# Performance work log

Measured on AMD Instinct MI355X. Metric: run time of the kernel, lower is better.

The kernel has to match this reference:

```python
import jax, jax.numpy as jnp
import numpy as np

# Problem sizes
B, NPG, K = 64, 1024, 16          # graphs, nodes-per-graph, kNN neighbors
IN_CH, OUT_CH, SPACE, PROP = 64, 128, 4, 64
N = B * NPG


def setup_inputs() -> dict:
    key = jax.random.key(0)
    ks = jax.random.split(key, 10)

    def lin(k, out_d, in_d):
        return jax.random.normal(k, (out_d, in_d), jnp.float32) / np.sqrt(in_d)

    x = jax.random.normal(ks[0], (N, IN_CH), jnp.float32)
    z = jax.random.normal(ks[1], (N,), jnp.float32)
    batch = (jnp.arange(N) // NPG).astype(jnp.int32)  # 64 equal graphs
    return {
        "x": x,
        "z": z,
        "batch": batch,
        "Ws": lin(ks[2], SPACE, IN_CH),
        "bs": jnp.zeros((SPACE,), jnp.float32),
        "Wh": lin(ks[3], PROP, IN_CH),
        "bh": jnp.zeros((PROP,), jnp.float32),
        "Wskip": lin(ks[4], OUT_CH, IN_CH),
        "Wagg": lin(ks[5], OUT_CH, 4 * PROP),
        "bagg": jnp.zeros((OUT_CH,), jnp.float32),
        "gamma": jnp.ones((OUT_CH,), jnp.float32),
        "beta": jnp.zeros((OUT_CH,), jnp.float32),
    }


def reference(x, z, batch, Ws, bs, Wh, bh, Wskip, Wagg, bagg, gamma, beta):
    # --- linear projections (torch Linear: y = x @ W.T + b) ---
    s = x @ Ws.T + bs                              # [N, SPACE] learned space
    h = x @ Wh.T + bh                              # [N, PROP]  propagated feats

    sB = s.reshape(B, NPG, SPACE)
    hB = h.reshape(B, NPG, PROP)
    zB = z.reshape(B, NPG)

    # --- exact kNN per graph (knn_graph with batch, no self-loops) ---
    sq = jnp.sum(sB * sB, -1)                      # [B, n]
    d2 = sq[:, :, None] + sq[:, None, :] - 2.0 * jnp.einsum("bnd,bmd->bnm", sB, sB)
    d2 = jnp.where(jnp.eye(NPG, dtype=bool), jnp.inf, d2)  # exclude self
    _, idx = jax.lax.top_k(-d2, K)                 # idx[b, i, :] = k nearest j
    idx = jax.lax.stop_gradient(idx)

    gather = jax.vmap(lambda a, i: a[i])           # per-graph row gather

    # --- edge weights ew = exp(-10 * ||s_src - s_dst||^2) ---
    s_nb = gather(sB, idx)                         # [B, n, K, SPACE]
    ew = jnp.exp(-10.0 * jnp.sum((s_nb - sB[:, :, None, :]) ** 2, -1))  # [B,n,K]

    # --- messages m = h[src] * ew ; each dst has exactly K incoming edges ---
    m = gather(hB, idx) * ew[..., None]            # [B, n, K, PROP]
    agg_mean = m.mean(axis=2)                      # scatter_mean
    agg_max = m.max(axis=2)                        # scatter_max

    # --- DGN directional aggregations over Z ---
    dz = gather(zB, idx) - zB[:, :, None]          # z[src] - z[dst], [B,n,K]
    dz_abs_sum = jnp.sum(jnp.abs(dz), axis=2)      # scatter_sum(|dz|), [B,n]
    F = dz / (dz_abs_sum[:, :, None] + 1e-8)       # [B, n, K]
    agg_smooth = (m * jnp.abs(F)[..., None]).mean(axis=2)
    agg_deriv = (m * F[..., None]).sum(axis=2)

    agg = jnp.concatenate([agg_mean, agg_max, agg_smooth, agg_deriv], -1)
    agg = agg.reshape(N, 4 * PROP)

    out = x @ Wskip.T + (agg @ Wagg.T + bagg)      # [N, OUT_CH]

    # --- BatchNorm1d (training-mode batch stats, biased var) + ReLU ---
    mu = out.mean(axis=0)
    var = out.var(axis=0)
    out = gamma * (out - mu) * jax.lax.rsqrt(var + 1e-5) + beta
    return jax.nn.relu(out)
```

## Files before the change

### kernel.cpp

```cpp
#include <hip/hip_runtime.h>
#include <hip/hip_bf16.h>
#include <math.h>

#define NPG   1024
#define KNN   16
#define IN_CH 64
#define OUT_CH 128
#define SPACE 4
#define PROP  64
#define NGRAPH 64
#define NTOT  (NGRAPH*NPG)

typedef unsigned long long u64;
typedef unsigned int u32;

#define K_INF ((0xFF800000ULL << 32) | 0x3FFULL)

__global__ __launch_bounds__(256) void k1_proj(
    const float* __restrict__ x, const float* __restrict__ Ws, const float* __restrict__ bs,
    const float* __restrict__ Wh, const float* __restrict__ bh,
    float* __restrict__ s_out, float* __restrict__ h_out)
{
    __shared__ float whl[PROP*IN_CH];
    __shared__ float wsl[SPACE*IN_CH];
    int tid = threadIdx.x;
    {
        const float4* src = (const float4*)Wh;
        float4* dst = (float4*)whl;
        for (int e = tid; e < PROP*IN_CH/4; e += 256) dst[e] = src[e];
        if (tid < SPACE*IN_CH/4) ((float4*)wsl)[tid] = ((const float4*)Ws)[tid];
    }
    __syncthreads();
    int i = blockIdx.x*256 + tid;

    float4 xr[16];
    const float4* xrow = (const float4*)(x + (size_t)i*IN_CH);
    #pragma unroll
    for (int q = 0; q < 16; q++) xr[q] = xrow[q];

    #pragma unroll
    for (int d = 0; d < SPACE; d++) {
        float acc = bs[d];
        const float4* wr = (const float4*)(wsl + d*IN_CH);
        #pragma unroll
        for (int q = 0; q < 16; q++) {
            float4 w = wr[q];
            acc += xr[q].x*w.x + xr[q].y*w.y + xr[q].z*w.z + xr[q].w*w.w;
        }
        s_out[(size_t)i*SPACE + d] = acc;
    }
    #pragma unroll 4
    for (int p = 0; p < PROP; p++) {
        float acc = bh[p];
        const float4* wr = (const float4*)(whl + p*IN_CH);
        #pragma unroll
        for (int q = 0; q < 16; q++) {
            float4 w = wr[q];
            acc += xr[q].x*w.x + xr[q].y*w.y + xr[q].z*w.z + xr[q].w*w.w;
        }
        h_out[(size_t)i*PROP + p] = acc;
    }
}

#define CEU(a,b) { u64 _lo=(a)<(b)?(a):(b); u64 _hi=(a)<(b)?(b):(a); (a)=_lo; (b)=_hi; }
#define CED(a,b) { u64 _lo=(a)<(b)?(a):(b); u64 _hi=(a)<(b)?(b):(a); (a)=_hi; (b)=_lo; }

#define M16N(n0,n1,n2,n3,n4,n5,n6,n7,n8,n9,n10,n11,n12,n13,n14,n15) \
 CEU(n0,n8) CEU(n1,n9) CEU(n2,n10) CEU(n3,n11) CEU(n4,n12) CEU(n5,n13) CEU(n6,n14) CEU(n7,n15) \
 CEU(n0,n4) CEU(n1,n5) CEU(n2,n6) CEU(n3,n7) CEU(n8,n12) CEU(n9,n13) CEU(n10,n14) CEU(n11,n15) \
 CEU(n0,n2) CEU(n1,n3) CEU(n4,n6) CEU(n5,n7) CEU(n8,n10) CEU(n9,n11) CEU(n12,n14) CEU(n13,n15) \
 CEU(n0,n1) CEU(n2,n3) CEU(n4,n5) CEU(n6,n7) CEU(n8,n9) CEU(n10,n11) CEU(n12,n13) CEU(n14,n15)

#define S16N(n0,n1,n2,n3,n4,n5,n6,n7,n8,n9,n10,n11,n12,n13,n14,n15) \
 CEU(n0,n1) CED(n2,n3) CEU(n4,n5) CED(n6,n7) CEU(n8,n9) CED(n10,n11) CEU(n12,n13) CED(n14,n15) \
 CEU(n0,n2) CEU(n1,n3) CED(n4,n6) CED(n5,n7) CEU(n8,n10) CEU(n9,n11) CED(n12,n14) CED(n13,n15) \
 CEU(n0,n1) CEU(n2,n3) CED(n4,n5) CED(n6,n7) CEU(n8,n9) CEU(n10,n11) CED(n12,n13) CED(n14,n15) \
 CEU(n0,n4) CEU(n1,n5) CEU(n2,n6) CEU(n3,n7) CED(n8,n12) CED(n9,n13) CED(n10,n14) CED(n11,n15) \
 CEU(n0,n2) CEU(n1,n3) CEU(n4,n6) CEU(n5,n7) CED(n8,n10) CED(n9,n11) CED(n12,n14) CED(n13,n15) \
 CEU(n0,n1) CEU(n2,n3) CED(n4,n5) CED(n6,n7) CEU(n8,n9) CEU(n10,n11) CED(n12,n13) CED(n14,n15) \
 M16N(n0,n1,n2,n3,n4,n5,n6,n7,n8,n9,n10,n11,n12,n13,n14,n15)

__device__ __forceinline__ float unmono(u32 uw) {
    return __uint_as_float((uw & 0x80000000u) ? (uw & 0x7FFFFFFFu) : ~uw);
}

#define POPN(b, dst) { \
    int _jb = (int)(q0 & 1023u); \
    q0 = (q0 >> 10) | (q1 << 54); q1 = (q1 >> 10) | (q2 << 54); q2 >>= 10; \
    float4 _sb = s4[_jb]; \
    float _dx = si.x-_sb.x, _dy = si.y-_sb.y, _dz = si.z-_sb.z, _dw = si.w-_sb.w; \
    float _db = _dx*_dx + _dy*_dy + _dz*_dz + _dw*_dw; \
    u32 _u = __float_as_uint(_db); _u = (_u >> 31) ? ~_u : (_u | 0x80000000u); \
    dst = ((b) < cnt) ? ((((u64)_u) << 32) | (u32)_jb) : ~0ULL; \
}

#define FLUSHK() do{ \
    u64 n0,n1,n2,n3,n4,n5,n6,n7,n8,n9,n10,n11,n12,n13,n14,n15; \
    POPN(0,n0) POPN(1,n1) POPN(2,n2) POPN(3,n3) POPN(4,n4) POPN(5,n5) POPN(6,n6) POPN(7,n7) \
    POPN(8,n8) POPN(9,n9) POPN(10,n10) POPN(11,n11) POPN(12,n12) POPN(13,n13) POPN(14,n14) POPN(15,n15) \
    S16N(n0,n1,n2,n3,n4,n5,n6,n7,n8,n9,n10,n11,n12,n13,n14,n15) \
    kk0 =kk0 <n15?kk0 :n15; kk1 =kk1 <n14?kk1 :n14; kk2 =kk2 <n13?kk2 :n13; kk3 =kk3 <n12?kk3 :n12; \
    kk4 =kk4 <n11?kk4 :n11; kk5 =kk5 <n10?kk5 :n10; kk6 =kk6 <n9 ?kk6 :n9 ; kk7 =kk7 <n8 ?kk7 :n8 ; \
    kk8 =kk8 <n7 ?kk8 :n7 ; kk9 =kk9 <n6 ?kk9 :n6 ; kk10=kk10<n5 ?kk10:n5 ; kk11=kk11<n4 ?kk11:n4 ; \
    kk12=kk12<n3 ?kk12:n3 ; kk13=kk13<n2 ?kk13:n2 ; kk14=kk14<n1 ?kk14:n1 ; kk15=kk15<n0 ?kk15:n0 ; \
    M16N(kk0,kk1,kk2,kk3,kk4,kk5,kk6,kk7,kk8,kk9,kk10,kk11,kk12,kk13,kk14,kk15) \
    cnt = 0; \
    wf = unmono((u32)(kk15 >> 32)); \
}while(0)

#define SHF64(v,mm) ((u64)__shfl_xor((long long)(v), (mm)))
#define MRG(mm) do{ \
    u64 p0=SHF64(kk15,mm), p1=SHF64(kk14,mm), p2 =SHF64(kk13,mm), p3 =SHF64(kk12,mm); \
    u64 p4=SHF64(kk11,mm), p5=SHF64(kk10,mm), p6 =SHF64(kk9,mm),  p7 =SHF64(kk8,mm); \
    u64 p8=SHF64(kk7,mm),  p9=SHF64(kk6,mm),  p10=SHF64(kk5,mm),  p11=SHF64(kk4,mm); \
    u64 p12=SHF64(kk3,mm), p13=SHF64(kk2,mm), p14=SHF64(kk1,mm),  p15=SHF64(kk0,mm); \
    kk0 =kk0 <p0 ?kk0 :p0 ; kk1 =kk1 <p1 ?kk1 :p1 ; kk2 =kk2 <p2 ?kk2 :p2 ; kk3 =kk3 <p3 ?kk3 :p3 ; \
    kk4 =kk4 <p4 ?kk4 :p4 ; kk5 =kk5 <p5 ?kk5 :p5 ; kk6 =kk6 <p6 ?kk6 :p6 ; kk7 =kk7 <p7 ?kk7 :p7 ; \
    kk8 =kk8 <p8 ?kk8 :p8 ; kk9 =kk9 <p9 ?kk9 :p9 ; kk10=kk10<p10?kk10:p10; kk11=kk11<p11?kk11:p11; \
    kk12=kk12<p12?kk12:p12; kk13=kk13<p13?kk13:p13; kk14=kk14<p14?kk14:p14; kk15=kk15<p15?kk15:p15; \
    M16N(kk0,kk1,kk2,kk3,kk4,kk5,kk6,kk7,kk8,kk9,kk10,kk11,kk12,kk13,kk14,kk15) \
}while(0)

#define OUTE(e, kv) if (((e) & 3) == r) { \
    int _j = (int)((kv) & 1023u); \
    float _d2 = unmono((u32)((kv) >> 32)); \
    ew_out[bq + (e)] = expf(-10.0f * _d2); \
    idx_out[bq + (e)] = gbase + _j; }

__attribute__((amdgpu_waves_per_eu(4, 4)))
__global__ __launch_bounds__(256) void k2_knn(
    const float* __restrict__ s, int* __restrict__ idx_out, float* __restrict__ ew_out)
{
    __shared__ float4 s4[NPG];
    int tid = threadIdx.x;
    int g    = blockIdx.x >> 4;
    int gbase = g * NPG;
    int qblk = (blockIdx.x & 15) * 64;
    const float4* sg = (const float4*)(s + (size_t)g*NPG*SPACE);
    for (int e = tid; e < NPG; e += 256) s4[e] = sg[e];
    __syncthreads();

    int lane = tid & 63;
    int grp  = lane >> 2;
    int r    = lane & 3;
    int q    = qblk + (tid >> 6)*16 + grp;
    float4 si = s4[q];

    u64 kk0=K_INF,kk1=K_INF,kk2=K_INF,kk3=K_INF,kk4=K_INF,kk5=K_INF,kk6=K_INF,kk7=K_INF,
        kk8=K_INF,kk9=K_INF,kk10=K_INF,kk11=K_INF,kk12=K_INF,kk13=K_INF,kk14=K_INF,kk15=K_INF;
    float wf = INFINITY;
    int cnt = 0;
    u64 q0 = 0, q1 = 0, q2 = 0;

    #pragma unroll 1
    for (int it = 0; it < 256; ++it) {
        int j = r*256 + ((it + 61*r) & 255);
        float4 sj = s4[j];
        float dx = si.x-sj.x, dy = si.y-sj.y, dz = si.z-sj.z, dw = si.w-sj.w;
        float d2 = dx*dx + dy*dy + dz*dz + dw*dw;
        if ((d2 <= wf) && (j != q)) {
            q2 = (q2 << 10) | (q1 >> 54);
            q1 = (q1 << 10) | (q0 >> 54);
            q0 = (q0 << 10) | (u32)j;
            cnt++;
        }
        if (__any(cnt >= 16)) FLUSHK();
    }
    if (__any(cnt > 0)) FLUSHK();

    MRG(1);
    MRG(2);

    size_t bq = ((size_t)(gbase + q)) * KNN;
    OUTE(0,kk0)  OUTE(1,kk1)  OUTE(2,kk2)  OUTE(3,kk3)
    OUTE(4,kk4)  OUTE(5,kk5)  OUTE(6,kk6)  OUTE(7,kk7)
    OUTE(8,kk8)  OUTE(9,kk9)  OUTE(10,kk10) OUTE(11,kk11)
    OUTE(12,kk12) OUTE(13,kk13) OUTE(14,kk14) OUTE(15,kk15)
}

typedef __attribute__((ext_vector_type(8))) short bf16x8;
typedef __attribute__((ext_vector_type(4))) float f32x4;

__device__ __forceinline__ u32 pk2bf(float a, float b) {
    u32 ua = __float_as_uint(a);
    u32 ub = __float_as_uint(b);
    ua = (ua + 0x7fffu + ((ua >> 16) & 1u)) >> 16;
    ub = (ub + 0x7fffu + ((ub >> 16) & 1u)) >> 16;
    return (ua & 0xffffu) | (ub << 16);
}
__device__ __forceinline__ unsigned short bfr(float a) {
    u32 ua = __float_as_uint(a);
    ua = (ua + 0x7fffu + ((ua >> 16) & 1u)) >> 16;
    return (unsigned short)ua;
}

__global__ __launch_bounds__(256) void k34_agg_gemm(
    const float* __restrict__ x, const float* __restrict__ h,
    const float* __restrict__ z, const int* __restrict__ idx,
    const float* __restrict__ ew,
    const float* __restrict__ Wskip, const float* __restrict__ Wagg,
    const float* __restrict__ bagg, float* __restrict__ out,
    float* __restrict__ partial)
{
    __shared__ char AggL[64*512];
    __shared__ char Bl[128*128];
    __shared__ float st[128], st2[128];
    int tid = threadIdx.x;
    int lane = tid & 63, wid = tid >> 6;
    int bid = blockIdx.x;
    int tile = (bid & 7) * 128 + (bid >> 3);
    int mbase = tile * 64;

    if (tid < 128) { st[tid] = 0.f; st2[tid] = 0.f; }

    #pragma unroll 2
    for (int t = 0; t < 16; ++t) {
        int row = wid*16 + t;
        int node = mbase + row;
        int kq = lane & 15;
        int jv = idx[(size_t)node*KNN + kq];
        float ev = ew[(size_t)node*KNN + kq];
        float dz = z[jv] - z[node];
        float as = fabsf(dz);
        as += __shfl_xor(as, 1); as += __shfl_xor(as, 2);
        as += __shfl_xor(as, 4); as += __shfl_xor(as, 8);
        float F = dz / (as + 1e-8f);
        float mean = 0.f, mx = -INFINITY, sm = 0.f, dv = 0.f;
        #pragma unroll
        for (int k = 0; k < KNN; ++k) {
            int   j = __shfl(jv, k);
            float e = __shfl(ev, k);
            float f = __shfl(F,  k);
            float hv = h[(size_t)j*PROP + lane];
            float m = hv * e;
            mean += m; mx = fmaxf(mx, m);
            sm += m * fabsf(f); dv += m * f;
        }
        int swz = (row & 7) << 4;
        char* rp = AggL + row*512;
        *(unsigned short*)(rp + ((2*(lane      )) ^ swz)) = bfr(mean * 0.0625f);
        *(unsigned short*)(rp + ((2*(lane +  64)) ^ swz)) = bfr(mx);
        *(unsigned short*)(rp + ((2*(lane + 128)) ^ swz)) = bfr(sm * 0.0625f);
        *(unsigned short*)(rp + ((2*(lane + 192)) ^ swz)) = bfr(dv);
    }

    int wy = wid >> 1, wx = wid & 1;
    int colb = wx*64 + (lane & 15);
    f32x4 acc[2][4];
    #pragma unroll
    for (int nc = 0; nc < 4; ++nc) {
        float bv = bagg[colb + nc*16];
        #pragma unroll
        for (int mr = 0; mr < 2; ++mr) acc[mr][nc] = (f32x4){bv, bv, bv, bv};
    }

    int brow = tid >> 1, bkq = (tid & 1) * 32;
    int bsw = (brow & 7) << 4;

    for (int ch = 0; ch < 5; ++ch) {
        __syncthreads();
        const float* bp = (ch == 0) ? (Wskip + (size_t)brow*64  + bkq)
                                    : (Wagg  + (size_t)brow*256 + (ch-1)*64 + bkq);
        #pragma unroll
        for (int g2 = 0; g2 < 4; ++g2) {
            float4 f0 = ((const float4*)bp)[2*g2], f1 = ((const float4*)bp)[2*g2+1];
            uint4 u = { pk2bf(f0.x,f0.y), pk2bf(f0.z,f0.w), pk2bf(f1.x,f1.y), pk2bf(f1.z,f1.w) };
            *(uint4*)(Bl + brow*128 + ((bkq*2 + g2*16) ^ bsw)) = u;
        }
        __syncthreads();

        #pragma unroll
        for (int ks = 0; ks < 2; ++ks) {
            int kb = ks*64 + ((lane >> 4) * 16);
            bf16x8 af[2], bfrg[4];
            if (ch == 0) {
                int ke = ks*32 + (lane >> 4)*8;
                #pragma unroll
                for (int mr = 0; mr < 2; ++mr) {
                    int row = mbase + wy*32 + mr*16 + (lane & 15);
                    const float* xp = x + (size_t)row*64 + ke;
                    float4 f0 = *(const float4*)xp, f1 = *(const float4*)(xp + 4);
                    union { u32 u[4]; bf16x8 v; } cv;
                    cv.u[0] = pk2bf(f0.x,f0.y); cv.u[1] = pk2bf(f0.z,f0.w);
                    cv.u[2] = pk2bf(f1.x,f1.y); cv.u[3] = pk2bf(f1.z,f1.w);
                    af[mr] = cv.v;
                }
            } else {
                #pragma unroll
                for (int mr = 0; mr < 2; ++mr) {
                    int row = wy*32 + mr*16 + (lane & 15);
                    af[mr] = *(const bf16x8*)(AggL + row*512 + (ch-1)*128
                                              + (kb ^ ((row & 7) << 4)));
                }
            }
            #pragma unroll
            for (int nc = 0; nc < 4; ++nc) {
                int n = wx*64 + nc*16 + (lane & 15);
                bfrg[nc] = *(const bf16x8*)(Bl + n*128 + (kb ^ ((n & 7) << 4)));
            }
            #pragma unroll
            for (int mr = 0; mr < 2; ++mr)
                #pragma unroll
                for (int nc = 0; nc < 4; ++nc)
                    acc[mr][nc] = __builtin_amdgcn_mfma_f32_16x16x32_bf16(
                        af[mr], bfrg[nc], acc[mr][nc], 0, 0, 0);
        }
    }

    float s1[4] = {0,0,0,0}, s2[4] = {0,0,0,0};
    #pragma unroll
    for (int mr = 0; mr < 2; ++mr) {
        int r0 = mbase + wy*32 + mr*16 + (lane >> 4)*4;
        #pragma unroll
        for (int nc = 0; nc < 4; ++nc) {
            int c = colb + nc*16;
            #pragma unroll
            for (int j = 0; j < 4; ++j) {
                float v = acc[mr][nc][j];
                out[(size_t)(r0 + j)*OUT_CH + c] = v;
                s1[nc] += v;
                s2[nc] += v*v;
            }
        }
    }
    #pragma unroll
    for (int nc = 0; nc < 4; ++nc) {
        s1[nc] += __shfl_xor(s1[nc], 16); s1[nc] += __shfl_xor(s1[nc], 32);
        s2[nc] += __shfl_xor(s2[nc], 16); s2[nc] += __shfl_xor(s2[nc], 32);
    }
    __syncthreads();
    if ((lane >> 4) == 0) {
        #pragma unroll
        for (int nc = 0; nc < 4; ++nc) {
            atomicAdd(&st[colb + nc*16],  s1[nc]);
            atomicAdd(&st2[colb + nc*16], s2[nc]);
        }
    }
    __syncthreads();
    if (tid < 128) {
        partial[(size_t)bid*256 + tid]       = st[tid];
        partial[(size_t)bid*256 + 128 + tid] = st2[tid];
    }
}

__global__ __launch_bounds__(256) void k5_red(
    const float* __restrict__ partial, float* __restrict__ sums)
{
    int c = threadIdx.x;
    int b0 = blockIdx.x * 32;
    float acc = 0.f;
    #pragma unroll 8
    for (int b = 0; b < 32; ++b)
        acc += partial[(size_t)(b0 + b)*256 + c];
    atomicAdd(&sums[c], acc);
}

__global__ __launch_bounds__(256) void k6_bn(
    float* __restrict__ out, const float* __restrict__ sums,
    const float* __restrict__ gamma, const float* __restrict__ beta)
{
    int f = blockIdx.x*256 + threadIdx.x;
    float4 v = *(float4*)(out + (size_t)f*4);
    int o0 = (f*4) & 127;
    const float invN = 1.f / (float)NTOT;
    float r[4] = {v.x, v.y, v.z, v.w};
    #pragma unroll
    for (int c = 0; c < 4; c++) {
        int o = o0 + c;
        float mu  = sums[o] * invN;
        float var = sums[128+o] * invN - mu*mu;
        float sc  = gamma[o] * rsqrtf(var + 1e-5f);
        float sh  = beta[o] - mu*sc;
        float y = r[c]*sc + sh;
        r[c] = y > 0.f ? y : 0.f;
    }
    *(float4*)(out + (size_t)f*4) = make_float4(r[0], r[1], r[2], r[3]);
}

extern "C" void kernel_launch(void* const* d_in, const int* in_sizes, int n_in,
                              void* d_out, int out_size, void* d_ws, size_t ws_size,
                              hipStream_t stream)
{
    (void)in_sizes; (void)n_in; (void)out_size; (void)ws_size;
    const float* x     = (const float*)d_in[0];
    const float* z     = (const float*)d_in[1];
    const float* Ws    = (const float*)d_in[3];
    const float* bs    = (const float*)d_in[4];
    const float* Wh    = (const float*)d_in[5];
    const float* bh    = (const float*)d_in[6];
    const float* Wskip = (const float*)d_in[7];
    const float* Wagg  = (const float*)d_in[8];
    const float* bagg  = (const float*)d_in[9];
    const float* gamma = (const float*)d_in[10];
    const float* beta  = (const float*)d_in[11];
    float* out = (float*)d_out;

    const size_t N = NTOT;
    float* ws   = (float*)d_ws;
    float* sbuf = ws;
    float* hbuf = sbuf + N*4;
    int*   idxb = (int*)(hbuf + N*64);
    float* ewb  = (float*)(idxb + N*16);
    float* part = ewb + N*16;
    float* sums = part + 1024*256;

    hipMemsetAsync(sums, 0, 256*sizeof(float), stream);
    k1_proj<<<NTOT/256, 256, 0, stream>>>(x, Ws, bs, Wh, bh, sbuf, hbuf);
    k2_knn <<<NGRAPH*16, 256, 0, stream>>>(sbuf, idxb, ewb);
    k34_agg_gemm<<<NTOT/64, 256, 0, stream>>>(x, hbuf, z, idxb, ewb,
                                              Wskip, Wagg, bagg, out, part);
    k5_red<<<32, 256, 0, stream>>>(part, sums);
    k6_bn <<<NTOT*OUT_CH/4/256, 256, 0, stream>>>(out, sums, gamma, beta);
}
```

Before: 315.4 us.

## Replace filtered bitonic top-k with 32-bit packed-key med3 insertion network

```diff
diff --git a/kernel.cpp b/kernel.cpp
--- a/kernel.cpp
+++ b/kernel.cpp
@@ -14,8 +14,6 @@
 typedef unsigned long long u64;
 typedef unsigned int u32;
 
-#define K_INF ((0xFF800000ULL << 32) | 0x3FFULL)
-
 __global__ __launch_bounds__(256) void k1_proj(
     const float* __restrict__ x, const float* __restrict__ Ws, const float* __restrict__ bs,
     const float* __restrict__ Wh, const float* __restrict__ bh,
@@ -62,120 +60,92 @@
     }
 }
 
-#define CEU(a,b) { u64 _lo=(a)<(b)?(a):(b); u64 _hi=(a)<(b)?(b):(a); (a)=_lo; (b)=_hi; }
-#define CED(a,b) { u64 _lo=(a)<(b)?(a):(b); u64 _hi=(a)<(b)?(b):(a); (a)=_hi; (b)=_lo; }
-
-#define M16N(n0,n1,n2,n3,n4,n5,n6,n7,n8,n9,n10,n11,n12,n13,n14,n15) \
- CEU(n0,n8) CEU(n1,n9) CEU(n2,n10) CEU(n3,n11) CEU(n4,n12) CEU(n5,n13) CEU(n6,n14) CEU(n7,n15) \
- CEU(n0,n4) CEU(n1,n5) CEU(n2,n6) CEU(n3,n7) CEU(n8,n12) CEU(n9,n13) CEU(n10,n14) CEU(n11,n15) \
- CEU(n0,n2) CEU(n1,n3) CEU(n4,n6) CEU(n5,n7) CEU(n8,n10) CEU(n9,n11) CEU(n12,n14) CEU(n13,n15) \
- CEU(n0,n1) CEU(n2,n3) CEU(n4,n5) CEU(n6,n7) CEU(n8,n9) CEU(n10,n11) CEU(n12,n13) CEU(n14,n15)
-
-#define S16N(n0,n1,n2,n3,n4,n5,n6,n7,n8,n9,n10,n11,n12,n13,n14,n15) \
- CEU(n0,n1) CED(n2,n3) CEU(n4,n5) CED(n6,n7) CEU(n8,n9) CED(n10,n11) CEU(n12,n13) CED(n14,n15) \
- CEU(n0,n2) CEU(n1,n3) CED(n4,n6) CED(n5,n7) CEU(n8,n10) CEU(n9,n11) CED(n12,n14) CED(n13,n15) \
- CEU(n0,n1) CEU(n2,n3) CED(n4,n5) CED(n6,n7) CEU(n8,n9) CEU(n10,n11) CED(n12,n13) CED(n14,n15) \
- CEU(n0,n4) CEU(n1,n5) CEU(n2,n6) CEU(n3,n7) CED(n8,n12) CED(n9,n13) CED(n10,n14) CED(n11,n15) \
- CEU(n0,n2) CEU(n1,n3) CEU(n4,n6) CEU(n5,n7) CED(n8,n10) CED(n9,n11) CED(n12,n14) CED(n13,n15) \
- CEU(n0,n1) CEU(n2,n3) CED(n4,n5) CED(n6,n7) CEU(n8,n9) CEU(n10,n11) CED(n12,n13) CED(n14,n15) \
- M16N(n0,n1,n2,n3,n4,n5,n6,n7,n8,n9,n10,n11,n12,n13,n14,n15)
-
-__device__ __forceinline__ float unmono(u32 uw) {
-    return __uint_as_float((uw & 0x80000000u) ? (uw & 0x7FFFFFFFu) : ~uw);
-}
-
-#define POPN(b, dst) { \
-    int _jb = (int)(q0 & 1023u); \
-    q0 = (q0 >> 10) | (q1 << 54); q1 = (q1 >> 10) | (q2 << 54); q2 >>= 10; \
-    float4 _sb = s4[_jb]; \
-    float _dx = si.x-_sb.x, _dy = si.y-_sb.y, _dz = si.z-_sb.z, _dw = si.w-_sb.w; \
-    float _db = _dx*_dx + _dy*_dy + _dz*_dz + _dw*_dw; \
-    u32 _u = __float_as_uint(_db); _u = (_u >> 31) ? ~_u : (_u | 0x80000000u); \
-    dst = ((b) < cnt) ? ((((u64)_u) << 32) | (u32)_jb) : ~0ULL; \
-}
-
-#define FLUSHK() do{ \
-    u64 n0,n1,n2,n3,n4,n5,n6,n7,n8,n9,n10,n11,n12,n13,n14,n15; \
-    POPN(0,n0) POPN(1,n1) POPN(2,n2) POPN(3,n3) POPN(4,n4) POPN(5,n5) POPN(6,n6) POPN(7,n7) \
-    POPN(8,n8) POPN(9,n9) POPN(10,n10) POPN(11,n11) POPN(12,n12) POPN(13,n13) POPN(14,n14) POPN(15,n15) \
-    S16N(n0,n1,n2,n3,n4,n5,n6,n7,n8,n9,n10,n11,n12,n13,n14,n15) \
-    kk0 =kk0 <n15?kk0 :n15; kk1 =kk1 <n14?kk1 :n14; kk2 =kk2 <n13?kk2 :n13; kk3 =kk3 <n12?kk3 :n12; \
-    kk4 =kk4 <n11?kk4 :n11; kk5 =kk5 <n10?kk5 :n10; kk6 =kk6 <n9 ?kk6 :n9 ; kk7 =kk7 <n8 ?kk7 :n8 ; \
-    kk8 =kk8 <n7 ?kk8 :n7 ; kk9 =kk9 <n6 ?kk9 :n6 ; kk10=kk10<n5 ?kk10:n5 ; kk11=kk11<n4 ?kk11:n4 ; \
-    kk12=kk12<n3 ?kk12:n3 ; kk13=kk13<n2 ?kk13:n2 ; kk14=kk14<n1 ?kk14:n1 ; kk15=kk15<n0 ?kk15:n0 ; \
-    M16N(kk0,kk1,kk2,kk3,kk4,kk5,kk6,kk7,kk8,kk9,kk10,kk11,kk12,kk13,kk14,kk15) \
-    cnt = 0; \
-    wf = unmono((u32)(kk15 >> 32)); \
+#define MED3(d, x, a, b) asm("v_med3_u32 %0, %1, %2, %3" : "=v"(d) : "v"(x), "v"(a), "v"(b))
+#define UMIN(a,b) ((a)<(b)?(a):(b))
+
+#define INS16(x) do{ \
+    u32 _x = (x); \
+    MED3(kk15, _x, kk14, kk15); MED3(kk14, _x, kk13, kk14); \
+    MED3(kk13, _x, kk12, kk13); MED3(kk12, _x, kk11, kk12); \
+    MED3(kk11, _x, kk10, kk11); MED3(kk10, _x, kk9,  kk10); \
+    MED3(kk9,  _x, kk8,  kk9 ); MED3(kk8,  _x, kk7,  kk8 ); \
+    MED3(kk7,  _x, kk6,  kk7 ); MED3(kk6,  _x, kk5,  kk6 ); \
+    MED3(kk5,  _x, kk4,  kk5 ); MED3(kk4,  _x, kk3,  kk4 ); \
+    MED3(kk3,  _x, kk2,  kk3 ); MED3(kk2,  _x, kk1,  kk2 ); \
+    MED3(kk1,  _x, kk0,  kk1 ); kk0 = UMIN(_x, kk0); \
 }while(0)
 
-#define SHF64(v,mm) ((u64)__shfl_xor((long long)(v), (mm)))
-#define MRG(mm) do{ \
-    u64 p0=SHF64(kk15,mm), p1=SHF64(kk14,mm), p2 =SHF64(kk13,mm), p3 =SHF64(kk12,mm); \
-    u64 p4=SHF64(kk11,mm), p5=SHF64(kk10,mm), p6 =SHF64(kk9,mm),  p7 =SHF64(kk8,mm); \
-    u64 p8=SHF64(kk7,mm),  p9=SHF64(kk6,mm),  p10=SHF64(kk5,mm),  p11=SHF64(kk4,mm); \
-    u64 p12=SHF64(kk3,mm), p13=SHF64(kk2,mm), p14=SHF64(kk1,mm),  p15=SHF64(kk0,mm); \
-    kk0 =kk0 <p0 ?kk0 :p0 ; kk1 =kk1 <p1 ?kk1 :p1 ; kk2 =kk2 <p2 ?kk2 :p2 ; kk3 =kk3 <p3 ?kk3 :p3 ; \
-    kk4 =kk4 <p4 ?kk4 :p4 ; kk5 =kk5 <p5 ?kk5 :p5 ; kk6 =kk6 <p6 ?kk6 :p6 ; kk7 =kk7 <p7 ?kk7 :p7 ; \
-    kk8 =kk8 <p8 ?kk8 :p8 ; kk9 =kk9 <p9 ?kk9 :p9 ; kk10=kk10<p10?kk10:p10; kk11=kk11<p11?kk11:p11; \
-    kk12=kk12<p12?kk12:p12; kk13=kk13<p13?kk13:p13; kk14=kk14<p14?kk14:p14; kk15=kk15<p15?kk15:p15; \
-    M16N(kk0,kk1,kk2,kk3,kk4,kk5,kk6,kk7,kk8,kk9,kk10,kk11,kk12,kk13,kk14,kk15) \
+#define CEU32(a,b) { u32 _lo = UMIN(a,b); u32 _hi = (a)<(b)?(b):(a); (a)=_lo; (b)=_hi; }
+#define M16U(n0,n1,n2,n3,n4,n5,n6,n7,n8,n9,n10,n11,n12,n13,n14,n15) \
+ CEU32(n0,n8) CEU32(n1,n9) CEU32(n2,n10) CEU32(n3,n11) CEU32(n4,n12) CEU32(n5,n13) CEU32(n6,n14) CEU32(n7,n15) \
+ CEU32(n0,n4) CEU32(n1,n5) CEU32(n2,n6) CEU32(n3,n7) CEU32(n8,n12) CEU32(n9,n13) CEU32(n10,n14) CEU32(n11,n15) \
+ CEU32(n0,n2) CEU32(n1,n3) CEU32(n4,n6) CEU32(n5,n7) CEU32(n8,n10) CEU32(n9,n11) CEU32(n12,n14) CEU32(n13,n15) \
+ CEU32(n0,n1) CEU32(n2,n3) CEU32(n4,n5) CEU32(n6,n7) CEU32(n8,n9) CEU32(n10,n11) CEU32(n12,n13) CEU32(n14,n15)
+
+#define MRGU(mm) do{ \
+    u32 p0 =(u32)__shfl_xor((int)kk15,mm), p1 =(u32)__shfl_xor((int)kk14,mm); \
+    u32 p2 =(u32)__shfl_xor((int)kk13,mm), p3 =(u32)__shfl_xor((int)kk12,mm); \
+    u32 p4 =(u32)__shfl_xor((int)kk11,mm), p5 =(u32)__shfl_xor((int)kk10,mm); \
+    u32 p6 =(u32)__shfl_xor((int)kk9, mm), p7 =(u32)__shfl_xor((int)kk8, mm); \
+    u32 p8 =(u32)__shfl_xor((int)kk7, mm), p9 =(u32)__shfl_xor((int)kk6, mm); \
+    u32 p10=(u32)__shfl_xor((int)kk5, mm), p11=(u32)__shfl_xor((int)kk4, mm); \
+    u32 p12=(u32)__shfl_xor((int)kk3, mm), p13=(u32)__shfl_xor((int)kk2, mm); \
+    u32 p14=(u32)__shfl_xor((int)kk1, mm), p15=(u32)__shfl_xor((int)kk0, mm); \
+    kk0 =UMIN(kk0 ,p0 ); kk1 =UMIN(kk1 ,p1 ); kk2 =UMIN(kk2 ,p2 ); kk3 =UMIN(kk3 ,p3 ); \
+    kk4 =UMIN(kk4 ,p4 ); kk5 =UMIN(kk5 ,p5 ); kk6 =UMIN(kk6 ,p6 ); kk7 =UMIN(kk7 ,p7 ); \
+    kk8 =UMIN(kk8 ,p8 ); kk9 =UMIN(kk9 ,p9 ); kk10=UMIN(kk10,p10); kk11=UMIN(kk11,p11); \
+    kk12=UMIN(kk12,p12); kk13=UMIN(kk13,p13); kk14=UMIN(kk14,p14); kk15=UMIN(kk15,p15); \
+    M16U(kk0,kk1,kk2,kk3,kk4,kk5,kk6,kk7,kk8,kk9,kk10,kk11,kk12,kk13,kk14,kk15) \
 }while(0)
 
-#define OUTE(e, kv) if (((e) & 3) == r) { \
+#define OUTE8(e, kv) if (((e) & 7) == r) { \
     int _j = (int)((kv) & 1023u); \
-    float _d2 = unmono((u32)((kv) >> 32)); \
+    float4 _sj = s4[_j]; \
+    float _dx = si.x-_sj.x, _dy = si.y-_sj.y, _dz = si.z-_sj.z, _dw = si.w-_sj.w; \
+    float _d2 = _dx*_dx + _dy*_dy + _dz*_dz + _dw*_dw; \
     ew_out[bq + (e)] = expf(-10.0f * _d2); \
     idx_out[bq + (e)] = gbase + _j; }
 
-__attribute__((amdgpu_waves_per_eu(4, 4)))
 __global__ __launch_bounds__(256) void k2_knn(
     const float* __restrict__ s, int* __restrict__ idx_out, float* __restrict__ ew_out)
 {
     __shared__ float4 s4[NPG];
     int tid = threadIdx.x;
-    int g    = blockIdx.x >> 4;
+    int g     = blockIdx.x >> 5;
     int gbase = g * NPG;
-    int qblk = (blockIdx.x & 15) * 64;
+    int qblk  = (blockIdx.x & 31) * 32;
     const float4* sg = (const float4*)(s + (size_t)g*NPG*SPACE);
     for (int e = tid; e < NPG; e += 256) s4[e] = sg[e];
     __syncthreads();
 
     int lane = tid & 63;
-    int grp  = lane >> 2;
-    int r    = lane & 3;
-    int q    = qblk + (tid >> 6)*16 + grp;
+    int grp  = lane >> 3;
+    int r    = lane & 7;
+    int q    = qblk + (tid >> 6)*8 + grp;
     float4 si = s4[q];
 
-    u64 kk0=K_INF,kk1=K_INF,kk2=K_INF,kk3=K_INF,kk4=K_INF,kk5=K_INF,kk6=K_INF,kk7=K_INF,
-        kk8=K_INF,kk9=K_INF,kk10=K_INF,kk11=K_INF,kk12=K_INF,kk13=K_INF,kk14=K_INF,kk15=K_INF;
-    float wf = INFINITY;
-    int cnt = 0;
-    u64 q0 = 0, q1 = 0, q2 = 0;
-
-    #pragma unroll 1
-    for (int it = 0; it < 256; ++it) {
-        int j = r*256 + ((it + 61*r) & 255);
+    u32 kk0=~0u,kk1=~0u,kk2=~0u,kk3=~0u,kk4=~0u,kk5=~0u,kk6=~0u,kk7=~0u,
+        kk8=~0u,kk9=~0u,kk10=~0u,kk11=~0u,kk12=~0u,kk13=~0u,kk14=~0u,kk15=~0u;
+
+    int jb0 = r*128;
+    #pragma unroll 2
+    for (int it = 0; it < 128; ++it) {
+        int j = jb0 + ((it + 3*r) & 127);
         float4 sj = s4[j];
         float dx = si.x-sj.x, dy = si.y-sj.y, dz = si.z-sj.z, dw = si.w-sj.w;
         float d2 = dx*dx + dy*dy + dz*dz + dw*dw;
-        if ((d2 <= wf) && (j != q)) {
-            q2 = (q2 << 10) | (q1 >> 54);
-            q1 = (q1 << 10) | (q0 >> 54);
-            q0 = (q0 << 10) | (u32)j;
-            cnt++;
-        }
-        if (__any(cnt >= 16)) FLUSHK();
-    }
-    if (__any(cnt > 0)) FLUSHK();
-
-    MRG(1);
-    MRG(2);
+        u32 key = (__float_as_uint(d2) & ~1023u) | (u32)j;
+        key = (j == q) ? ~0u : key;
+        INS16(key);
+    }
+
+    MRGU(1); MRGU(2); MRGU(4);
 
     size_t bq = ((size_t)(gbase + q)) * KNN;
-    OUTE(0,kk0)  OUTE(1,kk1)  OUTE(2,kk2)  OUTE(3,kk3)
-    OUTE(4,kk4)  OUTE(5,kk5)  OUTE(6,kk6)  OUTE(7,kk7)
-    OUTE(8,kk8)  OUTE(9,kk9)  OUTE(10,kk10) OUTE(11,kk11)
-    OUTE(12,kk12) OUTE(13,kk13) OUTE(14,kk14) OUTE(15,kk15)
+    OUTE8(0,kk0)  OUTE8(1,kk1)  OUTE8(2,kk2)   OUTE8(3,kk3)
+    OUTE8(4,kk4)  OUTE8(5,kk5)  OUTE8(6,kk6)   OUTE8(7,kk7)
+    OUTE8(8,kk8)  OUTE8(9,kk9)  OUTE8(10,kk10) OUTE8(11,kk11)
+    OUTE8(12,kk12) OUTE8(13,kk13) OUTE8(14,kk14) OUTE8(15,kk15)
 }
 
 typedef __attribute__((ext_vector_type(8))) short bf16x8;
@@ -406,7 +376,7 @@
 
     hipMemsetAsync(sums, 0, 256*sizeof(float), stream);
     k1_proj<<<NTOT/256, 256, 0, stream>>>(x, Ws, bs, Wh, bh, sbuf, hbuf);
-    k2_knn <<<NGRAPH*16, 256, 0, stream>>>(sbuf, idxb, ewb);
+    k2_knn <<<NGRAPH*32, 256, 0, stream>>>(sbuf, idxb, ewb);
     k34_agg_gemm<<<NTOT/64, 256, 0, stream>>>(x, hbuf, z, idxb, ewb,
                                               Wskip, Wagg, bagg, out, part);
     k5_red<<<32, 256, 0, stream>>>(part, sums);
```

Measured after the change: 269.0 us. -14.7%, faster.
